# Kernel tuning notes

Hardware: AMD Instinct MI355X
Metric: run time of the kernel (lower is better)

The kernel has to match this reference:

```python
import jax, jax.numpy as jnp
import numpy as np

D_MODEL = 2048
N_HEADS = 16
HEAD_DIM = D_MODEL // N_HEADS
B, T = 4, 2048


def setup_inputs() -> dict:
    key = jax.random.key(0)
    ks = jax.random.split(key, 10)
    s = 1.0 / np.sqrt(D_MODEL)
    x = jax.random.normal(ks[0], (B, T, D_MODEL), dtype=jnp.float32)
    # causal additive mask, broadcastable to [B, H, T, T]
    neg = jnp.finfo(jnp.float32).min
    causal = jnp.triu(jnp.full((T, T), neg, dtype=jnp.float32), k=1)
    mask = causal[None, None, :, :]
    return {
        "x": x,
        "mask": mask,
        "Wq": jax.random.uniform(ks[1], (D_MODEL, D_MODEL), jnp.float32, -s, s),
        "bq": jax.random.uniform(ks[2], (D_MODEL,), jnp.float32, -s, s),
        "Wk": jax.random.uniform(ks[3], (D_MODEL, HEAD_DIM), jnp.float32, -s, s),
        "bk": jax.random.uniform(ks[4], (HEAD_DIM,), jnp.float32, -s, s),
        "Wv": jax.random.uniform(ks[5], (D_MODEL, HEAD_DIM), jnp.float32, -s, s),
        "bv": jax.random.uniform(ks[6], (HEAD_DIM,), jnp.float32, -s, s),
        "Wo": jax.random.uniform(ks[7], (D_MODEL, D_MODEL), jnp.float32, -s, s),
        "bo": jax.random.uniform(ks[8], (D_MODEL,), jnp.float32, -s, s),
    }


def reference(x, mask, Wq, bq, Wk, bk, Wv, bv, Wo, bo):
    Bb, Tt, _ = x.shape
    H, Dh = N_HEADS, HEAD_DIM
    scale = 1.0 / jnp.sqrt(jnp.float32(Dh))
    q = (x @ Wq + bq).reshape(Bb, Tt, H, Dh)          # [B,T,H,D]
    k = x @ Wk + bk                                    # [B,T,D] (single KV head)
    v = x @ Wv + bv                                    # [B,T,D]
    # scores: [B,H,T,T] — q heads against shared k
    attn = jnp.einsum("bthd,bsd->bhts", q, k) * scale
    attn = attn + mask
    attn = jax.nn.softmax(attn, axis=-1)
    out = jnp.einsum("bhts,bsd->bthd", attn, v).reshape(Bb, Tt, D_MODEL)
    return out @ Wo + bo
```

## Files before the change

### kernel.cpp

```cpp
#include <hip/hip_runtime.h>
#include <hip/hip_bf16.h>
#include <stdint.h>

#define DEV __device__ __forceinline__

typedef unsigned short u16;
typedef unsigned int u32;
typedef __bf16 bf16x8 __attribute__((ext_vector_type(8)));
typedef float f32x4 __attribute__((ext_vector_type(4)));
typedef u16 u16x4 __attribute__((ext_vector_type(4)));
typedef u32 u32x4 __attribute__((ext_vector_type(4)));

typedef __attribute__((address_space(1))) u32 u32_as1;
typedef __attribute__((address_space(3))) u32 u32_as3;

static constexpr int Bn = 4, Tn = 2048, Dm = 2048, Hn = 16, Dh = 128;
static constexpr int BT = Bn * Tn;
static constexpr int KVSTR = 256;
static constexpr float CL2 = 0.1275174147f;

#define VMCNT(n) asm volatile("s_waitcnt vmcnt(" #n ")" ::: "memory")
#define BARRIER() __builtin_amdgcn_s_barrier()

DEV u16 f2bf(float f) {
  u32 u = __builtin_bit_cast(u32, f);
  u += 0x7fffu + ((u >> 16) & 1u);
  return (u16)(u >> 16);
}
DEV u16 cvt_bf(float f) { return __builtin_bit_cast(u16, (__bf16)f); }
DEV u32 cvt_pk_bf16(float lo, float hi) {
  u32 r;
  asm("v_cvt_pk_bf16_f32 %0, %1, %2" : "=v"(r) : "v"(lo), "v"(hi));
  return r;
}
DEV float max3f(float a, float b, float c) {
  float d;
  asm("v_max3_f32 %0, %1, %2, %3" : "=v"(d) : "v"(a), "v"(b), "v"(c));
  return d;
}

DEV void gl2lds16(const void* g, void* l) {
  __builtin_amdgcn_global_load_lds((u32_as1*)(uintptr_t)g,
                                   (u32_as3*)(u32)(uintptr_t)l, 16, 0, 0);
}

__global__ __launch_bounds__(256) void k_cast_bf16(const float* __restrict__ in,
                                                   u16* __restrict__ out, int n4) {
  int i = blockIdx.x * 256 + threadIdx.x;
  int stride = gridDim.x * 256;
  for (; i < n4; i += stride) {
    f32x4 v = ((const f32x4*)in)[i];
    u16x4 o;
    o.x = f2bf(v.x); o.y = f2bf(v.y); o.z = f2bf(v.z); o.w = f2bf(v.w);
    ((u16x4*)out)[i] = o;
  }
}

__global__ __launch_bounds__(256) void k_transpose_cast(const float* __restrict__ in,
                                                        u16* __restrict__ out,
                                                        int R, int C) {
  __shared__ float t[32][33];
  const int r0 = blockIdx.y * 32, c0 = blockIdx.x * 32;
  const int x = threadIdx.x, y = threadIdx.y;
#pragma unroll
  for (int i = 0; i < 4; ++i)
    t[y + i * 8][x] = in[(size_t)(r0 + y + i * 8) * C + c0 + x];
  __syncthreads();
#pragma unroll
  for (int i = 0; i < 4; ++i)
    out[(size_t)(c0 + y + i * 8) * R + r0 + x] = f2bf(t[x][y + i * 8]);
}

__global__ __launch_bounds__(256) void k_transpose_v(const u16* __restrict__ in,
                                                     int inStride,
                                                     u16* __restrict__ out,
                                                     int R, int C) {
  __shared__ u16 t[32][34];
  const int r0 = blockIdx.y * 32, c0 = blockIdx.x * 32;
  const int x = threadIdx.x, y = threadIdx.y;
#pragma unroll
  for (int i = 0; i < 4; ++i)
    t[y + i * 8][x] = in[(size_t)(r0 + y + i * 8) * inStride + c0 + x];
  __syncthreads();
  const int sx = (((x & 7) >> 2) << 4) | (((x >> 3) & 3) << 2) | (x & 3);
#pragma unroll
  for (int i = 0; i < 4; ++i)
    out[(size_t)(c0 + y + i * 8) * R + r0 + x] = t[sx][y + i * 8];
}

__global__ void k_concat_bias(const float* __restrict__ a, const float* __restrict__ b,
                              float* __restrict__ dst) {
  int i = threadIdx.x;
  dst[i] = (i < 128) ? a[i] : b[i - 128];
}

template <typename OutT>
__global__ __launch_bounds__(256) void k_gemm_bt(const u16* __restrict__ A,
                                                 const u16* __restrict__ Bt,
                                                 const float* __restrict__ bias,
                                                 OutT* __restrict__ C,
                                                 int M, int N, int K) {
  __shared__ __align__(128) char smem[32768];
  char* As = smem;
  char* Bs = smem + 16384;
  const int tid = threadIdx.x;
  const int wid = tid >> 6, lane = tid & 63;
  const int g = lane >> 4, r = lane & 15;
  const int wr = wid >> 1, wc = wid & 1;
  const int m0 = blockIdx.x * 128, n0 = blockIdx.y * 128;

  f32x4 acc[4][4];
#pragma unroll
  for (int m = 0; m < 4; ++m)
#pragma unroll
    for (int n = 0; n < 4; ++n) acc[m][n] = (f32x4)(0.f);

  for (int k0 = 0; k0 < K; k0 += 64) {
#pragma unroll
    for (int n = 0; n < 4; ++n) {
      const int L = n * 4096 + tid * 16;
      const int row = L >> 7;
      const int colb = (L & 127) ^ ((row & 7) << 4);
      gl2lds16((const char*)A + ((size_t)(m0 + row) * K + k0) * 2 + colb, As + L);
      gl2lds16((const char*)Bt + ((size_t)(n0 + row) * K + k0) * 2 + colb, Bs + L);
    }
    __syncthreads();
#pragma unroll
    for (int kk = 0; kk < 2; ++kk) {
      bf16x8 a[4], b[4];
#pragma unroll
      for (int m = 0; m < 4; ++m) {
        const int row = wr * 64 + m * 16 + r;
        a[m] = *(const bf16x8*)(As + row * 128 + ((kk * 64 + g * 16) ^ ((row & 7) << 4)));
      }
#pragma unroll
      for (int n = 0; n < 4; ++n) {
        const int row = wc * 64 + n * 16 + r;
        b[n] = *(const bf16x8*)(Bs + row * 128 + ((kk * 64 + g * 16) ^ ((row & 7) << 4)));
      }
#pragma unroll
      for (int m = 0; m < 4; ++m)
#pragma unroll
        for (int n = 0; n < 4; ++n)
          acc[m][n] = __builtin_amdgcn_mfma_f32_16x16x32_bf16(a[m], b[n], acc[m][n], 0, 0, 0);
    }
    __syncthreads();
  }

#pragma unroll
  for (int n = 0; n < 4; ++n) {
    const int col = n0 + wc * 64 + n * 16 + r;
    const float bv = bias[col];
#pragma unroll
    for (int m = 0; m < 4; ++m) {
#pragma unroll
      for (int j = 0; j < 4; ++j) {
        const int grow = m0 + wr * 64 + m * 16 + 4 * g + j;
        const float v = acc[m][n][j] + bv;
        if constexpr (sizeof(OutT) == 2)
          ((u16*)C)[(size_t)grow * N + col] = f2bf(v);
        else
          ((float*)C)[(size_t)grow * N + col] = v;
      }
    }
  }
}

template <typename OutT>
__global__ __launch_bounds__(512, 2) void k_gemm256(const u16* __restrict__ A,
                                                    const u16* __restrict__ Bt,
                                                    const float* __restrict__ bias,
                                                    OutT* __restrict__ C,
                                                    int M, int N, int K,
                                                    float oscale) {
  extern __shared__ char smem[];
  const int tid = threadIdx.x;
  const int wid = tid >> 6, lane = tid & 63;
  const int g = lane >> 4, r = lane & 15;
  const int wm = wid >> 2, wn = wid & 3;

  const int nbn = N >> 8;
  const int cpx = gridDim.x >> 3;
  const int linear = (blockIdx.x & 7) * cpx + (blockIdx.x >> 3);
  const int m0 = (linear / nbn) << 8;
  const int n0 = (linear % nbn) << 8;

  const int rowInCh = lane >> 3;
  const int colb = ((lane & 7) << 4) ^ (rowInCh << 4);
  const char* srcA0; const char* srcA1; const char* srcA2; const char* srcA3;
  const char* srcB0; const char* srcB1; const char* srcB2; const char* srcB3;
  int ldsA[4], ldsB[4];
  {
    const int wnh = (wid >> 1) & 1;
    const int cbb = ((wid >> 2) << 1) | (wid & 1);
    const char* sa[4]; const char* sb[4];
#pragma unroll
    for (int i = 0; i < 4; ++i) {
      const int chA = ((wid & 3) << 2) + i;
      const int lrA = (wm << 7) + (chA << 3) + rowInCh;
      sa[i] = (const char*)A + ((size_t)(m0 + lrA) * K) * 2 + colb;
      ldsA[i] = ((wm << 7) + (chA << 3)) * 128 + lane * 16;
      const int chB = (cbb << 2) + i;
      const int lrB = (wnh << 7) + (chB << 3) + rowInCh;
      sb[i] = (const char*)Bt + ((size_t)(n0 + lrB) * K) * 2 + colb;
      ldsB[i] = 32768 + ((wnh << 7) + (chB << 3)) * 128 + lane * 16;
    }
    srcA0 = sa[0]; srcA1 = sa[1]; srcA2 = sa[2]; srcA3 = sa[3];
    srcB0 = sb[0]; srcB1 = sb[1]; srcB2 = sb[2]; srcB3 = sb[3];
  }

  auto stage = [&](int t, int b) {
    const size_t ko = (size_t)t * 128;
    char* base = smem + (b << 16);
    gl2lds16(srcA0 + ko, base + ldsA[0]);
    gl2lds16(srcA1 + ko, base + ldsA[1]);
    gl2lds16(srcA2 + ko, base + ldsA[2]);
    gl2lds16(srcA3 + ko, base + ldsA[3]);
    gl2lds16(srcB0 + ko, base + ldsB[0]);
    gl2lds16(srcB1 + ko, base + ldsB[1]);
    gl2lds16(srcB2 + ko, base + ldsB[2]);
    gl2lds16(srcB3 + ko, base + ldsB[3]);
  };

  f32x4 acc[8][4];
#pragma unroll
  for (int m = 0; m < 8; ++m)
#pragma unroll
    for (int n = 0; n < 4; ++n) acc[m][n] = (f32x4)(0.f);

  auto readA = [&](const char* Ab, int qm, bf16x8 (&a)[8]) {
#pragma unroll
    for (int m = 0; m < 4; ++m) {
      const int row = (wm << 7) + ((qm * 4 + m) << 4) + r;
#pragma unroll
      for (int kk = 0; kk < 2; ++kk)
        a[m * 2 + kk] = *(const bf16x8*)(Ab + row * 128 + ((kk * 64 + g * 16) ^ ((row & 7) << 4)));
    }
  };
  auto readB = [&](const char* Bb, int qn, bf16x8 (&b)[4]) {
#pragma unroll
    for (int n = 0; n < 2; ++n) {
      const int row = (wn << 6) + ((qn * 2 + n) << 4) + r;
#pragma unroll
      for (int kk = 0; kk < 2; ++kk)
        b[n * 2 + kk] = *(const bf16x8*)(Bb + row * 128 + ((kk * 64 + g * 16) ^ ((row & 7) << 4)));
    }
  };
  auto mfmaQ = [&](const bf16x8 (&a)[8], const bf16x8 (&b)[4], int qm, int qn) {
    __builtin_amdgcn_s_setprio(1);
#pragma unroll
    for (int m = 0; m < 4; ++m)
#pragma unroll
      for (int n = 0; n < 2; ++n)
#pragma unroll
        for (int kk = 0; kk < 2; ++kk)
          acc[qm * 4 + m][qn * 2 + n] = __builtin_amdgcn_mfma_f32_16x16x32_bf16(
              a[m * 2 + kk], b[n * 2 + kk], acc[qm * 4 + m][qn * 2 + n], 0, 0, 0);
    __builtin_amdgcn_s_setprio(0);
  };

  const int NT = K >> 6;
  stage(0, 0);
  stage(1, 1);
  VMCNT(8);
  BARRIER();

  bf16x8 a0[8], a1[8], b0[4], b1[4];
  for (int t = 0; t < NT; ++t) {
    const char* Ab = smem + ((t & 1) << 16);
    const char* Bb = Ab + 32768;
    readA(Ab, 0, a0);
    readB(Bb, 0, b0);
    BARRIER();
    mfmaQ(a0, b0, 0, 0);
    BARRIER();
    readB(Bb, 1, b1);
    BARRIER();
    mfmaQ(a0, b1, 0, 1);
    BARRIER();
    readA(Ab, 1, a1);
    BARRIER();
    mfmaQ(a1, b1, 1, 1);
    BARRIER();
    if (t + 2 < NT) {
      stage(t + 2, t & 1);
      mfmaQ(a1, b0, 1, 0);
      VMCNT(8);
    } else {
      mfmaQ(a1, b0, 1, 0);
      VMCNT(0);
    }
    BARRIER();
  }

#pragma unroll
  for (int n = 0; n < 4; ++n) {
    const int col = n0 + wn * 64 + n * 16 + r;
    const float bv = bias[col];
#pragma unroll
    for (int m = 0; m < 8; ++m) {
#pragma unroll
      for (int j = 0; j < 4; ++j) {
        const int grow = m0 + wm * 128 + m * 16 + 4 * g + j;
        const float v = (acc[m][n][j] + bv) * oscale;
        if constexpr (sizeof(OutT) == 2)
          ((u16*)C)[(size_t)grow * N + col] = cvt_bf(v);
        else
          ((float*)C)[(size_t)grow * N + col] = v;
      }
    }
  }
}

__global__ __launch_bounds__(256, 3) void k_attn(const u16* __restrict__ Q,
                                                 const u16* __restrict__ Kb,
                                                 const u16* __restrict__ VT,
                                                 u16* __restrict__ O) {
  __shared__ __align__(1024) char smem[49152];
  char* Vs = smem + 32768;

  const int tid = threadIdx.x;
  const int wq = tid >> 6, lane = tid & 63;
  const int g = lane >> 4, r = lane & 15;

  const int bid = blockIdx.x;
  const int xcd = bid & 7, ii = bid >> 3;
  const int b = xcd >> 1;
  const int h = ((xcd & 1) << 3) | (ii & 7);
  const int qt = 15 - (ii >> 3);
  const int ntot = 2 * qt + 2;

  const float DEFER = 8.0f;

  bf16x8 qf[2][4];
  f32x4 o[2][8];
  float mrow[2], lrow[2];

  const int qrow0 = b * Tn + qt * 128 + wq * 32;
  const int qmin = qt * 128 + wq * 32;

#pragma unroll
  for (int m2 = 0; m2 < 2; ++m2) {
#pragma unroll
    for (int c = 0; c < 4; ++c)
      qf[m2][c] = *(const bf16x8*)(Q + (size_t)(qrow0 + m2 * 16 + r) * Dm + h * Dh + c * 32 + g * 8);
#pragma unroll
    for (int c = 0; c < 8; ++c) o[m2][c] = (f32x4)(0.f);
    mrow[m2] = -1e30f; lrow[m2] = 0.f;
  }

  auto stageK = [&](int s0, char* dst) {
#pragma unroll
    for (int n = 0; n < 4; ++n) {
      const int L = n * 4096 + tid * 16;
      const int row = L >> 8;
      const int colb = (L & 255) ^ ((row & 7) << 4);
      gl2lds16((const char*)Kb + (size_t)(s0 + row) * (KVSTR * 2) + colb, dst + L);
    }
  };
  auto stageV = [&](int s0) {
#pragma unroll
    for (int n = 0; n < 4; ++n) {
      const int L = n * 4096 + tid * 16;
      const int row = L >> 7;
      const int colb = (L & 127) ^ ((row & 7) << 4);
      gl2lds16((const char*)VT + ((size_t)row * BT + s0) * 2 + colb, Vs + L);
    }
  };

  stageK(b * Tn, smem);
  VMCNT(0);
  BARRIER();

  int cur = 0;
  for (int t = 0; t < ntot; ++t) {
    const int s0 = b * Tn + t * 64;

    stageV(s0);
    {
      const int st1 = (t + 1 < ntot) ? t + 1 : 0;
      stageK(b * Tn + st1 * 64, smem + ((cur ^ 1) << 14));
    }

    const bool fullmask = (t * 64 >= qmin + 32);
    u32x4 pau[2][2];
    if (!fullmask) {
      const char* Kc = smem + (cur << 14);
      f32x4 sf[2][4];
      __builtin_amdgcn_s_setprio(1);
#pragma unroll
      for (int n = 0; n < 4; ++n) {
        f32x4 sa = (f32x4)(0.f), sb = (f32x4)(0.f);
#pragma unroll
        for (int c = 0; c < 4; ++c) {
          const int row = n * 16 + r;
          bf16x8 kf = *(const bf16x8*)(Kc + row * 256 + ((c * 64 + g * 16) ^ ((row & 7) << 4)));
          sa = __builtin_amdgcn_mfma_f32_16x16x32_bf16(kf, qf[0][c], sa, 0, 0, 0);
          sb = __builtin_amdgcn_mfma_f32_16x16x32_bf16(kf, qf[1][c], sb, 0, 0, 0);
        }
        sf[0][n] = sa; sf[1][n] = sb;
      }
      __builtin_amdgcn_s_setprio(0);
      if (t * 64 + 63 > qmin) {
#pragma unroll
        for (int m2 = 0; m2 < 2; ++m2) {
          const int q = qmin + m2 * 16 + r;
#pragma unroll
          for (int n = 0; n < 4; ++n)
#pragma unroll
            for (int j = 0; j < 4; ++j) {
              const int key = t * 64 + n * 16 + 4 * g + j;
              if (key > q) sf[m2][n][j] = -1e30f;
            }
        }
      }
      float vmax[2];
      bool need = false;
#pragma unroll
      for (int m2 = 0; m2 < 2; ++m2) {
        f32x4 t4;
#pragma unroll
        for (int j = 0; j < 4; ++j)
          t4[j] = fmaxf(max3f(sf[m2][0][j], sf[m2][1][j], sf[m2][2][j]), sf[m2][3][j]);
        float v = fmaxf(max3f(t4[0], t4[1], t4[2]), t4[3]);
        v = fmaxf(v, __shfl_xor(v, 16));
        v = fmaxf(v, __shfl_xor(v, 32));
        vmax[m2] = v;
        need = need || (v > mrow[m2] + DEFER);
      }
      if (__any(need)) {
#pragma unroll
        for (int m2 = 0; m2 < 2; ++m2) {
          const float mnew = fmaxf(mrow[m2], vmax[m2]);
          const float fac = __builtin_amdgcn_exp2f(mrow[m2] - mnew);
          mrow[m2] = mnew;
          lrow[m2] *= fac;
#pragma unroll
          for (int j = 0; j < 4; ++j) {
            const float fb = __shfl(fac, 20 * g + j);
#pragma unroll
            for (int c = 0; c < 8; ++c) o[m2][c][j] *= fb;
          }
        }
      }
#pragma unroll
      for (int m2 = 0; m2 < 2; ++m2) {
        float rs = 0.f;
#pragma unroll
        for (int n = 0; n < 4; ++n) {
          const float p0 = __builtin_amdgcn_exp2f(sf[m2][n][0] - mrow[m2]);
          const float p1 = __builtin_amdgcn_exp2f(sf[m2][n][1] - mrow[m2]);
          const float p2 = __builtin_amdgcn_exp2f(sf[m2][n][2] - mrow[m2]);
          const float p3 = __builtin_amdgcn_exp2f(sf[m2][n][3] - mrow[m2]);
          rs += (p0 + p1) + (p2 + p3);
          pau[m2][n >> 1][(n & 1) * 2]     = cvt_pk_bf16(p0, p1);
          pau[m2][n >> 1][(n & 1) * 2 + 1] = cvt_pk_bf16(p2, p3);
        }
        rs += __shfl_xor(rs, 16);
        rs += __shfl_xor(rs, 32);
        lrow[m2] += rs;
      }
    }

    VMCNT(4);
    BARRIER();

    if (!fullmask) {
      __builtin_amdgcn_s_setprio(1);
#pragma unroll
      for (int kk = 0; kk < 2; ++kk) {
        if (t * 64 + kk * 32 >= qmin + 32) continue;
        const bf16x8 pa0 = __builtin_bit_cast(bf16x8, pau[0][kk]);
        const bf16x8 pa1 = __builtin_bit_cast(bf16x8, pau[1][kk]);
#pragma unroll
        for (int c = 0; c < 8; ++c) {
          const int row = c * 16 + r;
          const bf16x8 vb = *(const bf16x8*)(Vs + row * 128 + ((kk * 64 + g * 16) ^ ((row & 7) << 4)));
          o[0][c] = __builtin_amdgcn_mfma_f32_16x16x32_bf16(pa0, vb, o[0][c], 0, 0, 0);
          o[1][c] = __builtin_amdgcn_mfma_f32_16x16x32_bf16(pa1, vb, o[1][c], 0, 0, 0);
        }
      }
      __builtin_amdgcn_s_setprio(0);
    }

    VMCNT(0);
    BARRIER();
    cur ^= 1;
  }

#pragma unroll
  for (int m2 = 0; m2 < 2; ++m2) {
    float linv[4];
#pragma unroll
    for (int j = 0; j < 4; ++j)
      linv[j] = __builtin_amdgcn_rcpf(__shfl(lrow[m2], 20 * g + j));
#pragma unroll
    for (int c = 0; c < 8; ++c)
#pragma unroll
      for (int j = 0; j < 4; ++j)
        O[(size_t)(qrow0 + m2 * 16 + 4 * g + j) * Dm + h * Dh + c * 16 + r] =
            cvt_bf(o[m2][c][j] * linv[j]);
  }
}

extern "C" void kernel_launch(void* const* d_in, const int* in_sizes, int n_in,
                              void* d_out, int out_size, void* d_ws, size_t ws_size,
                              hipStream_t stream) {
  const float* x  = (const float*)d_in[0];
  const float* Wq = (const float*)d_in[2];
  const float* bq = (const float*)d_in[3];
  const float* Wk = (const float*)d_in[4];
  const float* bk = (const float*)d_in[5];
  const float* Wv = (const float*)d_in[6];
  const float* bv = (const float*)d_in[7];
  const float* Wo = (const float*)d_in[8];
  const float* bo = (const float*)d_in[9];
  float* out = (float*)d_out;

  char* ws = (char*)d_ws;
  size_t off = 0;
  auto alloc = [&](size_t bytes) {
    char* p = ws + off;
    off += (bytes + 255) & ~(size_t)255;
    return p;
  };
  u16* xb   = (u16*)alloc((size_t)BT * Dm * 2);
  u16* Qb   = (u16*)alloc((size_t)BT * Dm * 2);
  u16* KVb  = (u16*)alloc((size_t)BT * KVSTR * 2);
  u16* VTb  = (u16*)alloc((size_t)BT * Dh * 2);
  u16* Wqt  = (u16*)alloc((size_t)Dm * Dm * 2);
  u16* Wkvt = (u16*)alloc((size_t)Dm * KVSTR * 2);
  u16* Wot  = (u16*)alloc((size_t)Dm * Dm * 2);
  float* bkv = (float*)alloc(KVSTR * sizeof(float));
  u16* Ob   = xb;

  hipFuncSetAttribute(reinterpret_cast<const void*>(&k_gemm256<u16>),
                      hipFuncAttributeMaxDynamicSharedMemorySize, 131072);
  hipFuncSetAttribute(reinterpret_cast<const void*>(&k_gemm256<float>),
                      hipFuncAttributeMaxDynamicSharedMemorySize, 131072);

  k_cast_bf16<<<2048, 256, 0, stream>>>(x, xb, BT * Dm / 4);
  dim3 tb(32, 8);
  k_transpose_cast<<<dim3(Dm / 32, Dm / 32), tb, 0, stream>>>(Wq, Wqt, Dm, Dm);
  k_transpose_cast<<<dim3(Dh / 32, Dm / 32), tb, 0, stream>>>(Wk, Wkvt, Dm, Dh);
  k_transpose_cast<<<dim3(Dh / 32, Dm / 32), tb, 0, stream>>>(Wv, Wkvt + (size_t)Dh * Dm, Dm, Dh);
  k_transpose_cast<<<dim3(Dm / 32, Dm / 32), tb, 0, stream>>>(Wo, Wot, Dm, Dm);
  k_concat_bias<<<1, 256, 0, stream>>>(bk, bv, bkv);

  k_gemm256<u16><<<(BT / 256) * (Dm / 256), 512, 131072, stream>>>(xb, Wqt, bq, Qb, BT, Dm, Dm, CL2);
  k_gemm_bt<u16><<<dim3(BT / 128, KVSTR / 128), 256, 0, stream>>>(xb, Wkvt, bkv, KVb, BT, KVSTR, Dm);
  k_transpose_v<<<dim3(Dh / 32, BT / 32), tb, 0, stream>>>(KVb + Dh, KVSTR, VTb, BT, Dh);

  k_attn<<<1024, 256, 0, stream>>>(Qb, KVb, VTb, Ob);

  k_gemm256<float><<<(BT / 256) * (Dm / 256), 512, 131072, stream>>>(Ob, Wot, bo, out, BT, Dm, Dm, 1.0f);
}
```

Baseline: 326.6 us.

## Pair causal query tiles per block and load K directly into registers

Each attention block now processes two query tiles (p and 15-p) back to back, so every block does the same causal work, and the grid is halved to 512 blocks. K fragments are loaded straight from global memory into registers instead of being staged through LDS, and V is double-buffered in LDS. The next tile's K/V loads are issued after the QK MFMAs so they overlap the softmax and PV work, with one wait and barrier per iteration. The aim is to remove causal load imbalance and LDS traffic for K, in exchange for higher register pressure (launch bounds dropped from 3 to 2 blocks per CU) and fewer resident blocks.

After: 421.9 us. 1.29x slower.

```diff
diff --git a/kernel.cpp b/kernel.cpp
--- a/kernel.cpp
+++ b/kernel.cpp
@@ -312,12 +312,11 @@
   }
 }
 
-__global__ __launch_bounds__(256, 3) void k_attn(const u16* __restrict__ Q,
+__global__ __launch_bounds__(256, 2) void k_attn(const u16* __restrict__ Q,
                                                  const u16* __restrict__ Kb,
                                                  const u16* __restrict__ VT,
                                                  u16* __restrict__ O) {
-  __shared__ __align__(1024) char smem[49152];
-  char* Vs = smem + 32768;
+  __shared__ __align__(1024) char smem[32768];
 
   const int tid = threadIdx.x;
   const int wq = tid >> 6, lane = tid & 63;
@@ -326,82 +325,117 @@
   const int bid = blockIdx.x;
   const int xcd = bid & 7, ii = bid >> 3;
   const int b = xcd >> 1;
-  const int h = ((xcd & 1) << 3) | (ii & 7);
-  const int qt = 15 - (ii >> 3);
-  const int ntot = 2 * qt + 2;
+  const int h = ((xcd & 1) << 3) | (ii >> 3);
+  const int p = ii & 7;
+  const int qtA = p, qtB = 15 - p;
+  const int nstA = 2 * qtA + 2;
+  const int ntot = nstA + 2 * qtB + 2;
 
   const float DEFER = 8.0f;
 
   bf16x8 qf[2][4];
+  bf16x8 kf[4][4];
   f32x4 o[2][8];
   float mrow[2], lrow[2];
 
-  const int qrow0 = b * Tn + qt * 128 + wq * 32;
-  const int qmin = qt * 128 + wq * 32;
-
-#pragma unroll
-  for (int m2 = 0; m2 < 2; ++m2) {
-#pragma unroll
-    for (int c = 0; c < 4; ++c)
-      qf[m2][c] = *(const bf16x8*)(Q + (size_t)(qrow0 + m2 * 16 + r) * Dm + h * Dh + c * 32 + g * 8);
-#pragma unroll
-    for (int c = 0; c < 8; ++c) o[m2][c] = (f32x4)(0.f);
-    mrow[m2] = -1e30f; lrow[m2] = 0.f;
-  }
-
-  auto stageK = [&](int s0, char* dst) {
-#pragma unroll
-    for (int n = 0; n < 4; ++n) {
-      const int L = n * 4096 + tid * 16;
-      const int row = L >> 8;
-      const int colb = (L & 255) ^ ((row & 7) << 4);
-      gl2lds16((const char*)Kb + (size_t)(s0 + row) * (KVSTR * 2) + colb, dst + L);
-    }
-  };
-  auto stageV = [&](int s0) {
+  auto loadQ = [&](int qrow0) {
+#pragma unroll
+    for (int m2 = 0; m2 < 2; ++m2)
+#pragma unroll
+      for (int c = 0; c < 4; ++c)
+        qf[m2][c] = *(const bf16x8*)(Q + (size_t)(qrow0 + m2 * 16 + r) * Dm + h * Dh + c * 32 + g * 8);
+  };
+  auto resetAcc = [&]() {
+#pragma unroll
+    for (int m2 = 0; m2 < 2; ++m2) {
+#pragma unroll
+      for (int c = 0; c < 8; ++c) o[m2][c] = (f32x4)(0.f);
+      mrow[m2] = -1e30f; lrow[m2] = 0.f;
+    }
+  };
+  auto storeO = [&](int qrow0) {
+#pragma unroll
+    for (int m2 = 0; m2 < 2; ++m2) {
+      float linv[4];
+#pragma unroll
+      for (int j = 0; j < 4; ++j)
+        linv[j] = __builtin_amdgcn_rcpf(__shfl(lrow[m2], 20 * g + j));
+#pragma unroll
+      for (int c = 0; c < 8; ++c)
+#pragma unroll
+        for (int j = 0; j < 4; ++j)
+          O[(size_t)(qrow0 + m2 * 16 + 4 * g + j) * Dm + h * Dh + c * 16 + r] =
+              cvt_bf(o[m2][c][j] * linv[j]);
+    }
+  };
+  auto issueK = [&](int s0) {
+#pragma unroll
+    for (int n = 0; n < 4; ++n)
+#pragma unroll
+      for (int c = 0; c < 4; ++c)
+        kf[n][c] = *(const bf16x8*)(Kb + (size_t)(s0 + n * 16 + r) * KVSTR + c * 32 + g * 8);
+  };
+  auto stageV = [&](int s0, char* dst) {
 #pragma unroll
     for (int n = 0; n < 4; ++n) {
       const int L = n * 4096 + tid * 16;
       const int row = L >> 7;
       const int colb = (L & 127) ^ ((row & 7) << 4);
-      gl2lds16((const char*)VT + ((size_t)row * BT + s0) * 2 + colb, Vs + L);
-    }
-  };
-
-  stageK(b * Tn, smem);
-  VMCNT(0);
-  BARRIER();
-
-  int cur = 0;
+      gl2lds16((const char*)VT + ((size_t)row * BT + s0) * 2 + colb, dst + L);
+    }
+  };
+
+  int qt = qtA;
+  int qrow0 = b * Tn + qt * 128 + wq * 32;
+  int qmin = qt * 128 + wq * 32;
+  loadQ(qrow0);
+  resetAcc();
+  issueK(b * Tn);
+  stageV(b * Tn, smem);
+
   for (int t = 0; t < ntot; ++t) {
-    const int s0 = b * Tn + t * 64;
-
-    stageV(s0);
-    {
-      const int st1 = (t + 1 < ntot) ? t + 1 : 0;
-      stageK(b * Tn + st1 * 64, smem + ((cur ^ 1) << 14));
-    }
-
-    const bool fullmask = (t * 64 >= qmin + 32);
+    VMCNT(0);
+    BARRIER();
+
+    if (t == nstA) {
+      storeO(qrow0);
+      qt = qtB;
+      qrow0 = b * Tn + qt * 128 + wq * 32;
+      qmin = qt * 128 + wq * 32;
+      loadQ(qrow0);
+      resetAcc();
+    }
+    const int st = (t < nstA) ? t : t - nstA;
+    const char* Vb = smem + ((t & 1) << 14);
+    char* Vnext = smem + (((t + 1) & 1) << 14);
+
+    const bool fullmask = (st * 64 >= qmin + 32);
     u32x4 pau[2][2];
+    f32x4 sf[2][4];
     if (!fullmask) {
-      const char* Kc = smem + (cur << 14);
-      f32x4 sf[2][4];
       __builtin_amdgcn_s_setprio(1);
 #pragma unroll
       for (int n = 0; n < 4; ++n) {
         f32x4 sa = (f32x4)(0.f), sb = (f32x4)(0.f);
 #pragma unroll
         for (int c = 0; c < 4; ++c) {
-          const int row = n * 16 + r;
-          bf16x8 kf = *(const bf16x8*)(Kc + row * 256 + ((c * 64 + g * 16) ^ ((row & 7) << 4)));
-          sa = __builtin_amdgcn_mfma_f32_16x16x32_bf16(kf, qf[0][c], sa, 0, 0, 0);
-          sb = __builtin_amdgcn_mfma_f32_16x16x32_bf16(kf, qf[1][c], sb, 0, 0, 0);
+          sa = __builtin_amdgcn_mfma_f32_16x16x32_bf16(kf[n][c], qf[0][c], sa, 0, 0, 0);
+          sb = __builtin_amdgcn_mfma_f32_16x16x32_bf16(kf[n][c], qf[1][c], sb, 0, 0, 0);
         }
         sf[0][n] = sa; sf[1][n] = sb;
       }
       __builtin_amdgcn_s_setprio(0);
-      if (t * 64 + 63 > qmin) {
+    }
+
+    {
+      const int t1 = t + 1;
+      const int st1 = (t1 >= ntot) ? 0 : ((t1 < nstA) ? t1 : t1 - nstA);
+      issueK(b * Tn + st1 * 64);
+      stageV(b * Tn + st1 * 64, Vnext);
+    }
+
+    if (!fullmask) {
+      if (st * 64 + 63 > qmin) {
 #pragma unroll
         for (int m2 = 0; m2 < 2; ++m2) {
           const int q = qmin + m2 * 16 + r;
@@ -409,7 +443,7 @@
           for (int n = 0; n < 4; ++n)
 #pragma unroll
             for (int j = 0; j < 4; ++j) {
-              const int key = t * 64 + n * 16 + 4 * g + j;
+              const int key = st * 64 + n * 16 + 4 * g + j;
               if (key > q) sf[m2][n][j] = -1e30f;
             }
         }
@@ -460,47 +494,25 @@
         rs += __shfl_xor(rs, 32);
         lrow[m2] += rs;
       }
-    }
-
-    VMCNT(4);
-    BARRIER();
-
-    if (!fullmask) {
+
       __builtin_amdgcn_s_setprio(1);
 #pragma unroll
       for (int kk = 0; kk < 2; ++kk) {
-        if (t * 64 + kk * 32 >= qmin + 32) continue;
+        if (st * 64 + kk * 32 >= qmin + 32) continue;
         const bf16x8 pa0 = __builtin_bit_cast(bf16x8, pau[0][kk]);
         const bf16x8 pa1 = __builtin_bit_cast(bf16x8, pau[1][kk]);
 #pragma unroll
         for (int c = 0; c < 8; ++c) {
           const int row = c * 16 + r;
-          const bf16x8 vb = *(const bf16x8*)(Vs + row * 128 + ((kk * 64 + g * 16) ^ ((row & 7) << 4)));
+          const bf16x8 vb = *(const bf16x8*)(Vb + row * 128 + ((kk * 64 + g * 16) ^ ((row & 7) << 4)));
           o[0][c] = __builtin_amdgcn_mfma_f32_16x16x32_bf16(pa0, vb, o[0][c], 0, 0, 0);
           o[1][c] = __builtin_amdgcn_mfma_f32_16x16x32_bf16(pa1, vb, o[1][c], 0, 0, 0);
         }
       }
       __builtin_amdgcn_s_setprio(0);
     }
-
-    VMCNT(0);
-    BARRIER();
-    cur ^= 1;
-  }
-
-#pragma unroll
-  for (int m2 = 0; m2 < 2; ++m2) {
-    float linv[4];
-#pragma unroll
-    for (int j = 0; j < 4; ++j)
-      linv[j] = __builtin_amdgcn_rcpf(__shfl(lrow[m2], 20 * g + j));
-#pragma unroll
-    for (int c = 0; c < 8; ++c)
-#pragma unroll
-      for (int j = 0; j < 4; ++j)
-        O[(size_t)(qrow0 + m2 * 16 + 4 * g + j) * Dm + h * Dh + c * 16 + r] =
-            cvt_bf(o[m2][c][j] * linv[j]);
-  }
+  }
+  storeO(qrow0);
 }
 
 extern "C" void kernel_launch(void* const* d_in, const int* in_sizes, int n_in,
@@ -551,7 +563,7 @@
   k_gemm_bt<u16><<<dim3(BT / 128, KVSTR / 128), 256, 0, stream>>>(xb, Wkvt, bkv, KVb, BT, KVSTR, Dm);
   k_transpose_v<<<dim3(Dh / 32, BT / 32), tb, 0, stream>>>(KVb + Dh, KVSTR, VTb, BT, Dh);
 
-  k_attn<<<1024, 256, 0, stream>>>(Qb, KVb, VTb, Ob);
+  k_attn<<<512, 256, 0, stream>>>(Qb, KVb, VTb, Ob);
 
   k_gemm256<float><<<(BT / 256) * (Dm / 256), 512, 131072, stream>>>(Ob, Wot, bo, out, BT, Dm, Dm, 1.0f);
 }
```
